# Optimization experiments

Hardware: AMD Instinct MI355X
Metric: run time of the kernel (lower is better)

Reference implementation:

```python
import jax, jax.numpy as jnp
import numpy as np
from jax import lax

H, W = 96, 96          # PNet output map size
STRIDE, CELL = 2, 12   # PNet stride / receptive cell
SCALE = 12.0 / 20.0    # first pyramid scale = net_size / min_face_size
THR_SCORE = 0.6        # threshold[0]
THR_NMS = 0.5          # per-scale NMS threshold in detect_pnet


def setup_inputs() -> dict:
    key = jax.random.key(0)
    k1, k2 = jax.random.split(key)
    cls_prob = jax.random.uniform(k1, (H, W), dtype=jnp.float32)
    bbox_pred = jax.random.normal(k2, (H, W, 4), dtype=jnp.float32) * 0.1
    return {"cls_prob": cls_prob, "bbox_pred": bbox_pred}


def _nms_keep(boxes, scores, mask, thr):
    """Greedy NMS over N boxes with validity mask; returns bool keep mask [N]."""
    N = scores.shape[0]
    # invalid boxes sort last
    order = jnp.argsort(-jnp.where(mask, scores, -jnp.inf))
    b = boxes[order]
    m = mask[order]
    x1, y1, x2, y2 = b[:, 0], b[:, 1], b[:, 2], b[:, 3]
    areas = (x2 - x1 + 1.0) * (y2 - y1 + 1.0)
    # pairwise IoU [N, N]
    xx1 = jnp.maximum(x1[:, None], x1[None, :])
    yy1 = jnp.maximum(y1[:, None], y1[None, :])
    xx2 = jnp.minimum(x2[:, None], x2[None, :])
    yy2 = jnp.minimum(y2[:, None], y2[None, :])
    inter = jnp.maximum(xx2 - xx1 + 1.0, 0.0) * jnp.maximum(yy2 - yy1 + 1.0, 0.0)
    iou = inter / (areas[:, None] + areas[None, :] - inter)
    idx = jnp.arange(N)

    def step(keep, xs):
        i, iou_row, m_i = xs
        suppressed = jnp.any(keep & (iou_row > thr) & (idx < i))
        k_i = m_i & jnp.logical_not(suppressed)
        keep = keep.at[i].set(k_i)
        return keep, None

    keep_sorted, _ = lax.scan(step, jnp.zeros((N,), bool), (idx, iou, m))
    return jnp.zeros((N,), bool).at[order].set(keep_sorted)


def reference(cls_prob, bbox_pred):
    # generate_bbox: decode grid anchors back to original-image coords
    rows, cols = jnp.meshgrid(jnp.arange(H, dtype=jnp.float32),
                              jnp.arange(W, dtype=jnp.float32), indexing="ij")
    x1 = jnp.round(STRIDE * cols / SCALE).reshape(-1)
    y1 = jnp.round(STRIDE * rows / SCALE).reshape(-1)
    x2 = jnp.round((STRIDE * cols + CELL) / SCALE).reshape(-1)
    y2 = jnp.round((STRIDE * rows + CELL) / SCALE).reshape(-1)
    score = cls_prob.reshape(-1)
    reg = bbox_pred.reshape(-1, 4)
    mask = score > THR_SCORE

    boxes5 = jnp.stack([x1, y1, x2, y2, score], axis=-1)  # [N,5]
    keep = _nms_keep(boxes5[:, :4], score, mask, THR_NMS)

    bbw = x2 - x1 + 1.0
    bbh = y2 - y1 + 1.0
    boxes_c = jnp.stack([x1 + reg[:, 0] * bbw,
                         y1 + reg[:, 1] * bbh,
                         x2 + reg[:, 2] * bbw,
                         y2 + reg[:, 3] * bbh,
                         score], axis=-1)  # [N,5]
    return boxes_c * keep[:, None].astype(boxes_c.dtype)
```

## Files before the change

### kernel.cpp

```cpp
#include <hip/hip_runtime.h>


namespace {

constexpr int Hh = 96, Ww = 96, Nn = Hh * Ww;
constexpr int NW = Nn / 64;
constexpr float THR_SCORE = 0.6f;
constexpr int NT = 512;


__device__ __forceinline__ unsigned long long shift_b(const unsigned long long w[9], int b) {
  switch (b) {
    case 0:  return (w[4] << 1)  | (w[3] >> 63);
    case 1:  return (w[4] >> 1)  | (w[5] << 63);
    case 2:  return (w[4] << 2)  | (w[3] >> 62);
    case 3:  return (w[4] >> 2)  | (w[5] << 62);
    case 4:  return (w[3] << 32) | (w[2] >> 32);
    case 5:  return (w[5] >> 32) | (w[6] << 32);
    case 6:  return w[1];
    case 7:  return w[7];
    case 8:  return (w[3] << 33) | (w[2] >> 31);
    case 9:  return (w[3] << 31) | (w[2] >> 33);
    case 10: return (w[5] >> 31) | (w[6] << 33);
    default: return (w[5] >> 33) | (w[6] << 31);
  }
}

__global__ __launch_bounds__(NT) void mtcnn_kernel(
    const float* __restrict__ cls,
    const float* __restrict__ bbox,
    float* __restrict__ out)
{
  __shared__ float s_sc[Nn];
  __shared__ unsigned long long s_D[12][NW];
  __shared__ unsigned long long s_Up[NW + 8];
  __shared__ unsigned long long s_Kp[NW + 8];
  __shared__ float s_lo[Ww], s_hi[Ww];
  __shared__ int s_ch[3];

  unsigned long long* const U = s_Up + 4;
  unsigned long long* const K = s_Kp + 4;

  const int tid = threadIdx.x;
  const int lane = tid & 63;
  const int OFF[12] = {-1, 1, -2, 2, -Ww, Ww, -2*Ww, 2*Ww, -Ww-1, -Ww+1, Ww-1, Ww+1};

  if (tid < Ww) {
    float c = (float)tid;
    s_lo[tid] = rintf((2.0f * c) / 0.6f);
    s_hi[tid] = rintf((2.0f * c + 12.0f) / 0.6f);
  }
  for (int q = tid; q < Nn / 4; q += NT)
    reinterpret_cast<float4*>(s_sc)[q] = reinterpret_cast<const float4*>(cls)[q];
  if (tid < 4) {
    s_Up[tid] = 0ull; s_Kp[tid] = 0ull;
    s_Up[4 + NW + tid] = 0ull; s_Kp[4 + NW + tid] = 0ull;
  }
  if (tid < 3) s_ch[tid] = 0;
  __syncthreads();

  for (int n = tid; n < Nn; n += NT) {
    float si = s_sc[n];
    unsigned int m = 0;
    bool valid = si > THR_SCORE;
    if (valid) {
      int r = n / Ww, c = n - r * Ww;
      int rm = r % 3, cm = c % 3;
      unsigned int geom = (1u << 0) | (1u << 1) | (1u << 4) | (1u << 5);
      if (cm == 1) geom |= 1u << 2;
      if (cm == 2) geom |= 1u << 3;
      if (rm == 1) geom |= 1u << 6;
      if (rm == 2) geom |= 1u << 7;
      if (!(rm == 2 && cm == 2)) geom |= 1u << 8;
      if (!(rm == 2 && cm == 1)) geom |= 1u << 9;
      if (!(rm == 1 && cm == 2)) geom |= 1u << 10;
      if (!(rm == 1 && cm == 1)) geom |= 1u << 11;
      unsigned int inb = 0;
      bool cge1 = c >= 1, cle = c <= Ww - 2, rge1 = r >= 1, rle = r <= Hh - 2;
      if (cge1) inb |= 1u << 0;
      if (cle)  inb |= 1u << 1;
      if (c >= 2)      inb |= 1u << 2;
      if (c <= Ww - 3) inb |= 1u << 3;
      if (rge1) inb |= 1u << 4;
      if (rle)  inb |= 1u << 5;
      if (r >= 2)      inb |= 1u << 6;
      if (r <= Hh - 3) inb |= 1u << 7;
      if (rge1 && cge1) inb |= 1u << 8;
      if (rge1 && cle)  inb |= 1u << 9;
      if (rle && cge1)  inb |= 1u << 10;
      if (rle && cle)   inb |= 1u << 11;
      unsigned int cand = geom & inb;
      #pragma unroll
      for (int b = 0; b < 12; ++b) {
        int j = n + OFF[b];
        j = min(max(j, 0), Nn - 1);
        float sj = s_sc[j];
        bool ge = (b == 0) | (b == 2) | (b == 4) | (b == 6) | (b == 8) | (b == 9);
        bool dom = ge ? (sj >= si) : (sj > si);
        if (((cand >> b) & 1u) && (sj > THR_SCORE) && dom) m |= 1u << b;
      }
    }
    int w = n >> 6;
    #pragma unroll
    for (int b = 0; b < 12; ++b) {
      unsigned long long bb = __ballot((m >> b) & 1u);
      if (lane == 0) s_D[b][w] = bb;
    }
    unsigned long long vb = __ballot(valid);
    if (lane == 0) { U[w] = vb; K[w] = 0ull; }
  }
  __syncthreads();

  for (int it = 0; it < 9999; ++it) {
    const int f = it % 3;
    if (tid == 0) s_ch[(it + 1) % 3] = 0;
    if (tid < NW) {
      const int t = tid;
      unsigned long long u = U[t];
      if (u) {
        unsigned long long wu[9], wk[9];
        #pragma unroll
        for (int j = 0; j < 9; ++j) { wu[j] = U[t - 4 + j]; wk[j] = K[t - 4 + j]; }
        unsigned long long anyK = 0ull, anyU = 0ull;
        #pragma unroll
        for (int b = 0; b < 12; ++b) {
          unsigned long long d = s_D[b][t];
          anyK |= shift_b(wk, b) & d;
          anyU |= shift_b(wu, b) & d;
        }
        unsigned long long u2 = u & anyU & ~anyK;
        if (u2 != u) {
          K[t] = wk[4] | (u & ~anyU & ~anyK);
          U[t] = u2;
          s_ch[f] = 1;
        }
      }
    }
    __syncthreads();
    if (s_ch[f] == 0) break;
  }

  for (int n = tid; n < Nn; n += NT) {
    int r = n / Ww, c = n - r * Ww;
    float x1 = s_lo[c], x2 = s_hi[c], y1 = s_lo[r], y2 = s_hi[r];
    float k = (float)((K[n >> 6] >> (n & 63)) & 1ull);
    float bbw = x2 - x1 + 1.0f, bbh = y2 - y1 + 1.0f;
    float4 reg = reinterpret_cast<const float4*>(bbox)[n];
    out[n * 5 + 0] = (x1 + reg.x * bbw) * k;
    out[n * 5 + 1] = (y1 + reg.y * bbh) * k;
    out[n * 5 + 2] = (x2 + reg.z * bbw) * k;
    out[n * 5 + 3] = (y2 + reg.w * bbh) * k;
    out[n * 5 + 4] = s_sc[n] * k;
  }
}

}

extern "C" void kernel_launch(void* const* d_in, const int* in_sizes, int n_in,
                              void* d_out, int out_size, void* d_ws, size_t ws_size,
                              hipStream_t stream) {
  const float* cls  = (const float*)d_in[0];
  const float* bbox = (const float*)d_in[1];
  float* out = (float*)d_out;
  hipLaunchKernelGGL(mtcnn_kernel, dim3(1), dim3(NT), 0, stream, cls, bbox, out);
}
```

Baseline: 84.68 us.

## Split NMS and epilogue into separate kernels with change-driven word skipping

Splits the work into two kernels. A single-block NMS kernel writes keep bitmasks to workspace. A multi-block epilogue kernel then computes the calibrated boxes in parallel across many CUs, where before one block did all of it. The fixed-point iteration now tracks per-word change masks and only recomputes words whose neighbours within ±3 words changed in the previous round, cutting LDS traffic per iteration. The cost is an extra kernel launch and a global round-trip for the keep mask, and the NMS block shrinks to 256 threads.

```diff
diff --git a/kernel.cpp b/kernel.cpp
--- a/kernel.cpp
+++ b/kernel.cpp
@@ -6,8 +6,8 @@
 constexpr int Hh = 96, Ww = 96, Nn = Hh * Ww;
 constexpr int NW = Nn / 64;
 constexpr float THR_SCORE = 0.6f;
-constexpr int NT = 512;
-
+constexpr int NTA = 256;
+constexpr int NTB = 256;
 
 __device__ __forceinline__ unsigned long long shift_b(const unsigned long long w[9], int b) {
   switch (b) {
@@ -26,17 +26,15 @@
   }
 }
 
-__global__ __launch_bounds__(NT) void mtcnn_kernel(
+__global__ __launch_bounds__(NTA) void nms_kernel(
     const float* __restrict__ cls,
-    const float* __restrict__ bbox,
-    float* __restrict__ out)
+    unsigned long long* __restrict__ keep_out)
 {
   __shared__ float s_sc[Nn];
   __shared__ unsigned long long s_D[12][NW];
   __shared__ unsigned long long s_Up[NW + 8];
   __shared__ unsigned long long s_Kp[NW + 8];
-  __shared__ float s_lo[Ww], s_hi[Ww];
-  __shared__ int s_ch[3];
+  __shared__ unsigned long long s_chg[2][5];
 
   unsigned long long* const U = s_Up + 4;
   unsigned long long* const K = s_Kp + 4;
@@ -45,21 +43,20 @@
   const int lane = tid & 63;
   const int OFF[12] = {-1, 1, -2, 2, -Ww, Ww, -2*Ww, 2*Ww, -Ww-1, -Ww+1, Ww-1, Ww+1};
 
-  if (tid < Ww) {
-    float c = (float)tid;
-    s_lo[tid] = rintf((2.0f * c) / 0.6f);
-    s_hi[tid] = rintf((2.0f * c + 12.0f) / 0.6f);
-  }
-  for (int q = tid; q < Nn / 4; q += NT)
+  for (int q = tid; q < Nn / 4; q += NTA)
     reinterpret_cast<float4*>(s_sc)[q] = reinterpret_cast<const float4*>(cls)[q];
   if (tid < 4) {
     s_Up[tid] = 0ull; s_Kp[tid] = 0ull;
     s_Up[4 + NW + tid] = 0ull; s_Kp[4 + NW + tid] = 0ull;
   }
-  if (tid < 3) s_ch[tid] = 0;
+  if (tid == 0) {
+    s_chg[0][0] = 0ull; s_chg[0][4] = 0ull;
+    s_chg[1][0] = 0ull; s_chg[1][4] = 0ull;
+    s_chg[1][1] = ~0ull; s_chg[1][2] = ~0ull; s_chg[1][3] = ~0ull;
+  }
   __syncthreads();
 
-  for (int n = tid; n < Nn; n += NT) {
+  for (int n = tid; n < Nn; n += NTA) {
     float si = s_sc[n];
     unsigned int m = 0;
     bool valid = si > THR_SCORE;
@@ -111,47 +108,71 @@
   }
   __syncthreads();
 
-  for (int it = 0; it < 9999; ++it) {
-    const int f = it % 3;
-    if (tid == 0) s_ch[(it + 1) % 3] = 0;
-    if (tid < NW) {
+  int cur = 0;
+  for (int it = 0; it < 5000; ++it) {
+    if (tid < 192) {
+      bool changed = false;
       const int t = tid;
-      unsigned long long u = U[t];
-      if (u) {
-        unsigned long long wu[9], wk[9];
-        #pragma unroll
-        for (int j = 0; j < 9; ++j) { wu[j] = U[t - 4 + j]; wk[j] = K[t - 4 + j]; }
-        unsigned long long anyK = 0ull, anyU = 0ull;
-        #pragma unroll
-        for (int b = 0; b < 12; ++b) {
-          unsigned long long d = s_D[b][t];
-          anyK |= shift_b(wk, b) & d;
-          anyU |= shift_b(wu, b) & d;
-        }
-        unsigned long long u2 = u & anyU & ~anyK;
-        if (u2 != u) {
-          K[t] = wk[4] | (u & ~anyU & ~anyK);
-          U[t] = u2;
-          s_ch[f] = 1;
+      if (t < NW) {
+        int sh = (t - 3) & 63;
+        int wlo = (t + 61) >> 6;
+        unsigned long long A = s_chg[cur ^ 1][wlo];
+        unsigned long long Bw = s_chg[cur ^ 1][wlo + 1];
+        unsigned long long win = sh ? ((A >> sh) | (Bw << (64 - sh))) : A;
+        if (win & 0x7Full) {
+          unsigned long long u = U[t];
+          if (u) {
+            unsigned long long wu[9], wk[9];
+            #pragma unroll
+            for (int j = 0; j < 9; ++j) { wu[j] = U[t - 4 + j]; wk[j] = K[t - 4 + j]; }
+            unsigned long long anyK = 0ull, anyU = 0ull;
+            #pragma unroll
+            for (int b = 0; b < 12; ++b) {
+              unsigned long long d = s_D[b][t];
+              anyK |= shift_b(wk, b) & d;
+              anyU |= shift_b(wu, b) & d;
+            }
+            unsigned long long u2 = u & anyU & ~anyK;
+            if (u2 != u) {
+              K[t] = wk[4] | (u & ~anyU & ~anyK);
+              U[t] = u2;
+              changed = true;
+            }
+          }
         }
       }
+      unsigned long long bb = __ballot(changed);
+      if (lane == 0) s_chg[cur][1 + (tid >> 6)] = bb;
     }
     __syncthreads();
-    if (s_ch[f] == 0) break;
+    if ((s_chg[cur][1] | s_chg[cur][2] | s_chg[cur][3]) == 0ull) break;
+    cur ^= 1;
   }
 
-  for (int n = tid; n < Nn; n += NT) {
-    int r = n / Ww, c = n - r * Ww;
-    float x1 = s_lo[c], x2 = s_hi[c], y1 = s_lo[r], y2 = s_hi[r];
-    float k = (float)((K[n >> 6] >> (n & 63)) & 1ull);
-    float bbw = x2 - x1 + 1.0f, bbh = y2 - y1 + 1.0f;
-    float4 reg = reinterpret_cast<const float4*>(bbox)[n];
-    out[n * 5 + 0] = (x1 + reg.x * bbw) * k;
-    out[n * 5 + 1] = (y1 + reg.y * bbh) * k;
-    out[n * 5 + 2] = (x2 + reg.z * bbw) * k;
-    out[n * 5 + 3] = (y2 + reg.w * bbh) * k;
-    out[n * 5 + 4] = s_sc[n] * k;
-  }
+  if (tid < NW) keep_out[tid] = K[tid];
+}
+
+__global__ __launch_bounds__(NTB) void epi_kernel(
+    const float* __restrict__ cls,
+    const float* __restrict__ bbox,
+    const unsigned long long* __restrict__ keep,
+    float* __restrict__ out)
+{
+  const int n = blockIdx.x * NTB + threadIdx.x;
+  const int r = n / Ww, c = n - r * Ww;
+  const float fc = (float)c, fr = (float)r;
+  const float x1 = rintf((2.0f * fc) / 0.6f);
+  const float x2 = rintf((2.0f * fc + 12.0f) / 0.6f);
+  const float y1 = rintf((2.0f * fr) / 0.6f);
+  const float y2 = rintf((2.0f * fr + 12.0f) / 0.6f);
+  const float k = (float)((keep[n >> 6] >> (n & 63)) & 1ull);
+  const float4 reg = reinterpret_cast<const float4*>(bbox)[n];
+  const float bbw = x2 - x1 + 1.0f, bbh = y2 - y1 + 1.0f;
+  out[n * 5 + 0] = (x1 + reg.x * bbw) * k;
+  out[n * 5 + 1] = (y1 + reg.y * bbh) * k;
+  out[n * 5 + 2] = (x2 + reg.z * bbw) * k;
+  out[n * 5 + 3] = (y2 + reg.w * bbh) * k;
+  out[n * 5 + 4] = cls[n] * k;
 }
 
 }
@@ -162,5 +183,8 @@
   const float* cls  = (const float*)d_in[0];
   const float* bbox = (const float*)d_in[1];
   float* out = (float*)d_out;
-  hipLaunchKernelGGL(mtcnn_kernel, dim3(1), dim3(NT), 0, stream, cls, bbox, out);
+  unsigned long long* keep = (unsigned long long*)d_ws;
+  hipLaunchKernelGGL(nms_kernel, dim3(1), dim3(NTA), 0, stream, cls, keep);
+  hipLaunchKernelGGL(epi_kernel, dim3(Nn / NTB), dim3(NTB), 0, stream,
+                     cls, bbox, keep, out);
 }
```

After: 95.29 us. +12.5%, slower.
